# Performance work log

Measured on AMD Instinct MI355X. Metric: run time of the kernel, lower is better.

The kernel has to match this reference:

```python
import jax, jax.numpy as jnp
import numpy as np

WH, WW = 8, 8          # window_size
NUM_HEADS = 16
DIM = 512
NW = 64                # windows per image (mask leading dim)
BATCH = 16             # images
N = WH * WW            # tokens per window


def _relative_position_index():
    coords = np.stack(np.meshgrid(np.arange(WH), np.arange(WW), indexing='ij'))  # (2,Wh,Ww)
    cf = coords.reshape(2, -1)                                                   # (2,N)
    rel = cf[:, :, None] - cf[:, None, :]                                        # (2,N,N)
    rel = rel.transpose(1, 2, 0).astype(np.int64)                                # (N,N,2)
    rel[:, :, 0] += WH - 1
    rel[:, :, 1] += WW - 1
    rel[:, :, 0] *= 2 * WW - 1
    return jnp.asarray(rel.sum(-1), dtype=jnp.int32)                             # (N,N)


def setup_inputs() -> dict:
    key = jax.random.key(0)
    ks = jax.random.split(key, 8)
    B_ = BATCH * NW
    x = jax.random.normal(ks[0], (B_, N, DIM), dtype=jnp.float32)
    # 0 / -100 additive shift-style mask (Swin uses -100.0 for masked pairs)
    mraw = jax.random.uniform(ks[1], (NW, N, N))
    mask = jnp.where(mraw < 0.15, jnp.float32(-100.0), jnp.float32(0.0))
    qkv_w = jax.random.normal(ks[2], (3 * DIM, DIM), dtype=jnp.float32) * (DIM ** -0.5)
    qkv_b = jnp.zeros((3 * DIM,), dtype=jnp.float32)
    proj_w = jax.random.normal(ks[3], (DIM, DIM), dtype=jnp.float32) * (DIM ** -0.5)
    proj_b = jnp.zeros((DIM,), dtype=jnp.float32)
    n_rel = (2 * WH - 1) * (2 * WW - 1)  # 225
    rpb_table = jax.random.normal(ks[4], (n_rel, NUM_HEADS), dtype=jnp.float32) * 0.02
    rel_index = _relative_position_index()
    return {"x": x, "mask": mask, "qkv_w": qkv_w, "qkv_b": qkv_b,
            "proj_w": proj_w, "proj_b": proj_b, "rpb_table": rpb_table,
            "rel_index": rel_index}


def reference(x, mask, qkv_w, qkv_b, proj_w, proj_b, rpb_table, rel_index):
    B_, n, C = x.shape
    H = NUM_HEADS
    hd = C // H
    scale = hd ** -0.5
    qkv = x @ qkv_w.T + qkv_b                       # (B_, N, 3C)
    qkv = qkv.reshape(B_, n, 3, H, hd)
    q = qkv[:, :, 0].transpose(0, 2, 1, 3) * scale  # (B_, H, N, hd)
    k = qkv[:, :, 1].transpose(0, 2, 1, 3)
    v = qkv[:, :, 2].transpose(0, 2, 1, 3)
    attn = jnp.einsum('bhnd,bhmd->bhnm', q, k)      # (B_, H, N, N)
    bias = rpb_table[rel_index.reshape(-1)].reshape(n, n, H).transpose(2, 0, 1)  # (H,N,N)
    attn = attn + bias[None]
    nW = mask.shape[0]
    attn = attn.reshape(B_ // nW, nW, H, n, n) + mask[None, :, None]
    attn = jax.nn.softmax(attn.reshape(B_, H, n, n), axis=-1)
    out = jnp.einsum('bhnm,bhmd->bhnd', attn, v)    # (B_, H, N, hd)
    out = out.transpose(0, 2, 1, 3).reshape(B_, n, C)
    return out @ proj_w.T + proj_b
```

## Files before the change

### kernel.cpp

```cpp
#include <hip/hip_runtime.h>
#include <hip/hip_bf16.h>

typedef unsigned short u16;
typedef __attribute__((ext_vector_type(8))) short bfrag;
typedef __attribute__((ext_vector_type(4))) float ffrag;

#define NWIN_TOT 1024
#define NTOK 64
#define CDIM 512
#define NHEAD 16
#define HDIM 32
#define NW 64

__device__ __forceinline__ u16 f2bf(float f) {
  union { float f; unsigned u; } v; v.f = f;
  unsigned r = v.u + 0x7fffu + ((v.u >> 16) & 1u);
  return (u16)(r >> 16);
}

__device__ __forceinline__ float bfhi2f(unsigned hi_bits) {
  union { unsigned u; float f; } v; v.u = hi_bits; return v.f;
}

__device__ __forceinline__ ffrag mfma16(bfrag a, bfrag b, ffrag c) {
  return __builtin_amdgcn_mfma_f32_16x16x32_bf16(a, b, c, 0, 0, 0);
}

__device__ __forceinline__ void gload16(const u16* src, u16* lds) {
  __builtin_amdgcn_global_load_lds(
      (const __attribute__((address_space(1))) unsigned int*)src,
      (__attribute__((address_space(3))) unsigned int*)lds, 16, 0, 0);
}

#define BAR() __builtin_amdgcn_s_barrier()
#define SCHED0() __builtin_amdgcn_sched_barrier(0)
#define VMW(n) do { asm volatile("s_waitcnt vmcnt(" #n ")" ::: "memory"); \
                    __builtin_amdgcn_sched_barrier(0); } while (0)

__global__ __launch_bounds__(256) void k_prep(const float* __restrict__ x,
                                              const float* __restrict__ qkv_w,
                                              const float* __restrict__ proj_w,
                                              const int*   __restrict__ rel_index,
                                              const float* __restrict__ rpb,
                                              const float* __restrict__ mask,
                                              u16* __restrict__ xb,
                                              u16* __restrict__ wq, u16* __restrict__ wp,
                                              u16* __restrict__ combB) {
  int i = blockIdx.x * 256 + threadIdx.x;
  if (i < 4194304) {
    int e = i * 8;
    const float4* xp = reinterpret_cast<const float4*>(x + e);
    float4 lo = xp[0], hi = xp[1];
    union { u16 u[8]; bfrag v; } pk;
    pk.u[0] = f2bf(lo.x); pk.u[1] = f2bf(lo.y); pk.u[2] = f2bf(lo.z); pk.u[3] = f2bf(lo.w);
    pk.u[4] = f2bf(hi.x); pk.u[5] = f2bf(hi.y); pk.u[6] = f2bf(hi.z); pk.u[7] = f2bf(hi.w);
    *reinterpret_cast<bfrag*>(xb + e) = pk.v;
    return;
  }
  i -= 4194304;
  if (i < 786432) { wq[i] = f2bf(qkv_w[i]); return; }
  i -= 786432;
  if (i < 262144) { wp[i] = f2bf(proj_w[i]); return; }
  i -= 262144;
  {
    int wh = i >> 12, rc = i & 4095;
    int w0 = wh >> 4, h = wh & 15;
    combB[i] = f2bf(rpb[rel_index[rc] * 16 + h] + mask[(w0 << 12) + rc]);
  }
}

#define MFMAQ(mh, nh, BARR) \
  _Pragma("unroll") for (int i_ = 0; i_ < 4; ++i_) \
  _Pragma("unroll") for (int n_ = 0; n_ < 2; ++n_) \
  _Pragma("unroll") for (int ks_ = 0; ks_ < 2; ++ks_) \
    acc[(mh)*4+i_][(nh)*2+n_] = mfma16(a_[i_*2+ks_], BARR[n_*2+ks_], acc[(mh)*4+i_][(nh)*2+n_]);

template<int EPI>
__global__ __launch_bounds__(512, 2) void k_gemm8(const u16* __restrict__ A,
                                                  const u16* __restrict__ W,
                                                  const float* __restrict__ bias,
                                                  u16* __restrict__ qws, u16* __restrict__ kws,
                                                  u16* __restrict__ vws,
                                                  float* __restrict__ out) {
  constexpr int NT = (EPI == 0) ? 6 : 2;
  constexpr int NWG = 256 * NT;
  extern __shared__ __align__(16) u16 smem[];

  const int bid = blockIdx.x;
  const int tile = (bid & 7) * (NWG >> 3) + (bid >> 3);
  const int bn = tile % NT, bm = tile / NT;
  const int brow = bm << 8, bcol = bn << 8;

  const int tid = threadIdx.x;
  const int wv = tid >> 6, lane = tid & 63, c15 = lane & 15, g = lane >> 4;
  const int wr = wv >> 2, wc = wv & 3;
  const int rowA0 = wr * 128 + c15;
  const int rowB0 = wc * 64 + c15;
  const ffrag zf = {0.f, 0.f, 0.f, 0.f};

  ffrag acc[8][4];
#pragma unroll
  for (int i = 0; i < 8; ++i)
#pragma unroll
    for (int n = 0; n < 4; ++n) acc[i][n] = zf;

  auto stage = [&](int t, int mat, int half) {
    u16* db = smem + ((t & 1) * 2 + mat) * 16384 + half * 8192;
    const u16* gsrc = mat ? W : A;
    const int gr0 = (mat ? bcol : brow) + half * 128;
#pragma unroll
    for (int l = 0; l < 2; ++l) {
      int e = l * 4096 + tid * 8;
      int r = e >> 6, cb = (e & 63) << 1;
      int scol = (cb ^ ((r & 7) << 4)) >> 1;
      gload16(gsrc + (size_t)(gr0 + r) * 512 + t * 64 + scol, db + e);
    }
  };

  stage(0, 0, 0); stage(0, 0, 1); stage(0, 1, 0); stage(0, 1, 1);
  stage(1, 0, 0); stage(1, 0, 1); stage(1, 1, 0); stage(1, 1, 1);
  VMW(8);
  BAR();

  bfrag b0_[4];
  {
    const char* B0_ = (const char*)(smem + 1 * 16384);
#pragma unroll
    for (int n = 0; n < 2; ++n) {
      int rb = rowB0 + n * 16;
#pragma unroll
      for (int ks = 0; ks < 2; ++ks)
        b0_[n * 2 + ks] = *(const bfrag*)(B0_ + rb * 128 + ((ks * 64 + g * 16) ^ ((rb & 7) << 4)));
    }
  }

  for (int t = 0; t < 8; ++t) {
    const char* As_ = (const char*)(smem + ((t & 1) * 2 + 0) * 16384);
    const char* Bs_ = (const char*)(smem + ((t & 1) * 2 + 1) * 16384);
    bfrag a_[8], b1_[4];

#pragma unroll
    for (int i = 0; i < 4; ++i) {
      int ra = rowA0 + i * 16;
#pragma unroll
      for (int ks = 0; ks < 2; ++ks)
        a_[i * 2 + ks] = *(const bfrag*)(As_ + ra * 128 + ((ks * 64 + g * 16) ^ ((ra & 7) << 4)));
    }
    BAR();
    __builtin_amdgcn_s_setprio(1);
    MFMAQ(0, 0, b0_);
    __builtin_amdgcn_s_setprio(0);
    BAR();

#pragma unroll
    for (int n = 0; n < 2; ++n) {
      int rb = rowB0 + 32 + n * 16;
#pragma unroll
      for (int ks = 0; ks < 2; ++ks)
        b1_[n * 2 + ks] = *(const bfrag*)(Bs_ + rb * 128 + ((ks * 64 + g * 16) ^ ((rb & 7) << 4)));
    }
    BAR();
    __builtin_amdgcn_s_setprio(1);
    MFMAQ(0, 1, b1_);
    __builtin_amdgcn_s_setprio(0);
    BAR();

#pragma unroll
    for (int i = 0; i < 4; ++i) {
      int ra = rowA0 + 64 + i * 16;
#pragma unroll
      for (int ks = 0; ks < 2; ++ks)
        a_[i * 2 + ks] = *(const bfrag*)(As_ + ra * 128 + ((ks * 64 + g * 16) ^ ((ra & 7) << 4)));
    }
    SCHED0();
    if (t + 2 < 8) { stage(t + 2, 1, 0); stage(t + 2, 1, 1); }
    BAR();
    __builtin_amdgcn_s_setprio(1);
    MFMAQ(1, 1, b1_);
    __builtin_amdgcn_s_setprio(0);
    BAR();

    if (t + 2 < 8) { stage(t + 2, 0, 0); stage(t + 2, 0, 1); }
    if (t < 6) { VMW(8); } else if (t == 6) { VMW(0); }
    BAR();
    __builtin_amdgcn_s_setprio(1);
    MFMAQ(1, 0, b0_);
    __builtin_amdgcn_s_setprio(0);
    if (t < 7) {
      const char* Bn_ = (const char*)(smem + (((t + 1) & 1) * 2 + 1) * 16384);
#pragma unroll
      for (int n = 0; n < 2; ++n) {
        int rb = rowB0 + n * 16;
#pragma unroll
        for (int ks = 0; ks < 2; ++ks)
          b0_[n * 2 + ks] = *(const bfrag*)(Bn_ + rb * 128 + ((ks * 64 + g * 16) ^ ((rb & 7) << 4)));
      }
    }
    BAR();
  }

  if (EPI == 0) {
    const int which = bn >> 1;
    const int head0 = (bn & 1) * 8;
    const int win0 = brow >> 6;
    const float s = (which == 0) ? 0.17677669529663687f : 1.0f;
    u16* lds16 = smem;

#pragma unroll
    for (int n = 0; n < 4; ++n) {
      int colc = wc * 64 + n * 16 + c15;
      float bz = bias[bcol + colc];
#pragma unroll
      for (int i = 0; i < 8; ++i) {
#pragma unroll
        for (int r = 0; r < 4; ++r) {
          int row = wr * 128 + i * 16 + g * 4 + r;
          int ch = ((colc >> 3) ^ (row & 31)) & 31;
          lds16[row * 256 + (colc & 7) + (ch << 3)] = f2bf((acc[i][n][r] + bz) * s);
        }
      }
    }
    __syncthreads();

    if (which < 2) {
      u16* dst = (which == 0) ? qws : kws;
#pragma unroll
      for (int it = 0; it < 16; ++it) {
        int G = it * 512 + tid;
        int win = G >> 11, rem = G & 2047;
        int hl = rem >> 8, rem2 = rem & 255;
        int tok = rem2 >> 2, d0 = (rem2 & 3) << 3;
        int row = win * 64 + tok, col = hl * 32 + d0;
        int ch = ((col >> 3) ^ (row & 31)) & 31;
        bfrag v = *(const bfrag*)(lds16 + row * 256 + (ch << 3));
        size_t o = ((size_t)((win0 + win) * NHEAD + head0 + hl) * NTOK + tok) * HDIM + d0;
        *(bfrag*)(dst + o) = v;
      }
    } else {
#pragma unroll
      for (int it = 0; it < 16; ++it) {
        int G = it * 512 + tid;
        int win = G >> 11, rem = G & 2047;
        int hl = rem >> 8, rem2 = rem & 255;
        int d = rem2 >> 3, tok0 = (rem2 & 7) << 3;
        int col = hl * 32 + d;
        union { u16 u[8]; bfrag v; } pk;
#pragma unroll
        for (int j = 0; j < 8; ++j) {
          int row = win * 64 + tok0 + j;
          int ch = ((col >> 3) ^ (row & 31)) & 31;
          pk.u[j] = lds16[row * 256 + (col & 7) + (ch << 3)];
        }
        size_t o = ((size_t)((win0 + win) * NHEAD + head0 + hl) * HDIM + d) * NTOK + tok0;
        *(bfrag*)(vws + o) = pk.v;
      }
    }
  } else {
#pragma unroll
    for (int n = 0; n < 4; ++n) {
      int c = bcol + wc * 64 + n * 16 + c15;
      float bz = bias[c];
      float* po = out + (size_t)(brow + wr * 128) * CDIM + c;
#pragma unroll
      for (int i = 0; i < 8; ++i)
#pragma unroll
        for (int r = 0; r < 4; ++r)
          po[(size_t)(i * 16 + g * 4 + r) * CDIM] = acc[i][n][r] + bz;
    }
  }
}

__global__ __launch_bounds__(256) void k_attn(const u16* __restrict__ qws,
                                              const u16* __restrict__ kws,
                                              const u16* __restrict__ vws,
                                              const u16* __restrict__ combB,
                                              u16* __restrict__ yws) {
  __shared__ __align__(16) u16 plds[4][NTOK * NTOK];
  const int tid = threadIdx.x, w = tid >> 6, lane = tid & 63;
  const int c15 = lane & 15, g = lane >> 4, g4 = g * 4;
  const int p = blockIdx.x * 4 + w;
  const int b = p >> 4, h = p & 15;

  const u16* qb_ = qws + (size_t)p * (NTOK * HDIM);
  const u16* kb_ = kws + (size_t)p * (NTOK * HDIM);
  bfrag qa[4], ka[4];
#pragma unroll
  for (int t = 0; t < 4; ++t) {
    qa[t] = *reinterpret_cast<const bfrag*>(qb_ + (t * 16 + c15) * HDIM + g * 8);
    ka[t] = *reinterpret_cast<const bfrag*>(kb_ + (t * 16 + c15) * HDIM + g * 8);
  }

  const u16* cB = combB + ((size_t)(((b & (NW - 1)) << 4) + h) << 12);
  u16* pl = plds[w];
  const ffrag zf = {0.f, 0.f, 0.f, 0.f};

#pragma unroll
  for (int it = 0; it < 4; ++it) {
    int row = it * 16 + c15;
    float l[4][4];
    float mx = -3.0e38f;
#pragma unroll
    for (int jt = 0; jt < 4; ++jt) {
      ffrag s = mfma16(ka[jt], qa[it], zf);
      uint2 cw = *reinterpret_cast<const uint2*>(cB + row * 64 + jt * 16 + g4);
      l[jt][0] = s[0] + bfhi2f(cw.x << 16);
      l[jt][1] = s[1] + bfhi2f(cw.x & 0xffff0000u);
      l[jt][2] = s[2] + bfhi2f(cw.y << 16);
      l[jt][3] = s[3] + bfhi2f(cw.y & 0xffff0000u);
      mx = fmaxf(mx, fmaxf(fmaxf(l[jt][0], l[jt][1]), fmaxf(l[jt][2], l[jt][3])));
    }
    mx = fmaxf(mx, __shfl_xor(mx, 16));
    mx = fmaxf(mx, __shfl_xor(mx, 32));
    float sum = 0.f;
#pragma unroll
    for (int jt = 0; jt < 4; ++jt)
#pragma unroll
      for (int r = 0; r < 4; ++r) {
        float e = __expf(l[jt][r] - mx);
        l[jt][r] = e;
        sum += e;
      }
    sum += __shfl_xor(sum, 16);
    sum += __shfl_xor(sum, 32);
    float inv = 1.0f / sum;
#pragma unroll
    for (int jt = 0; jt < 4; ++jt) {
      union { u16 u[4]; uint2 v; } pk;
#pragma unroll
      for (int r = 0; r < 4; ++r) pk.u[r] = f2bf(l[jt][r] * inv);
      int off = row * 64 + ((jt * 16 + g4) ^ ((row & 7) << 3));
      *reinterpret_cast<uint2*>(&pl[off]) = pk.v;
    }
  }
  __syncthreads();

  const u16* vb_ = vws + (size_t)p * (HDIM * NTOK);
  ffrag o0[4] = {zf, zf, zf, zf}, o1[4] = {zf, zf, zf, zf};
#pragma unroll
  for (int ks = 0; ks < 2; ++ks) {
    bfrag vf0 = *reinterpret_cast<const bfrag*>(vb_ + c15 * NTOK + ks * 32 + g * 8);
    bfrag vf1 = *reinterpret_cast<const bfrag*>(vb_ + (16 + c15) * NTOK + ks * 32 + g * 8);
#pragma unroll
    for (int i = 0; i < 4; ++i) {
      int prow = i * 16 + c15;
      bfrag pa = *reinterpret_cast<const bfrag*>(
          &pl[prow * 64 + ((ks * 32 + g * 8) ^ ((prow & 7) << 3))]);
      o0[i] = mfma16(pa, vf0, o0[i]);
      o1[i] = mfma16(pa, vf1, o1[i]);
    }
  }
  __syncthreads();

  u16* yl = &plds[0][0];
#pragma unroll
  for (int i = 0; i < 4; ++i)
#pragma unroll
    for (int r = 0; r < 4; ++r) {
      int tok = i * 16 + g4 + r;
      yl[tok * 136 + w * 32 + c15] = f2bf(o0[i][r]);
      yl[tok * 136 + w * 32 + 16 + c15] = f2bf(o1[i][r]);
    }
  __syncthreads();
  {
    const int b2 = blockIdx.x >> 2;
    const int h0 = (blockIdx.x * 4) & 15;
    int row = tid >> 2, seg = tid & 3;
    const u16* src = yl + row * 136 + seg * 32;
    u16* dst = yws + ((size_t)b2 * NTOK + row) * CDIM + h0 * HDIM + seg * 32;
    bfrag v0 = *(const bfrag*)(src);
    bfrag v1 = *(const bfrag*)(src + 8);
    bfrag v2 = *(const bfrag*)(src + 16);
    bfrag v3 = *(const bfrag*)(src + 24);
    *(bfrag*)(dst) = v0;
    *(bfrag*)(dst + 8) = v1;
    *(bfrag*)(dst + 16) = v2;
    *(bfrag*)(dst + 24) = v3;
  }
}

extern "C" void kernel_launch(void* const* d_in, const int* in_sizes, int n_in,
                              void* d_out, int out_size, void* d_ws, size_t ws_size,
                              hipStream_t stream) {
  const float* x      = (const float*)d_in[0];
  const float* mask   = (const float*)d_in[1];
  const float* qkv_w  = (const float*)d_in[2];
  const float* qkv_b  = (const float*)d_in[3];
  const float* proj_w = (const float*)d_in[4];
  const float* proj_b = (const float*)d_in[5];
  const float* rpb    = (const float*)d_in[6];
  const int*   rel    = (const int*)d_in[7];
  float* out = (float*)d_out;

  char* ws = (char*)d_ws;
  constexpr size_t SZ_QKV = (size_t)NWIN_TOT * NHEAD * NTOK * HDIM * 2;
  u16* qws = (u16*)(ws);
  u16* kws = (u16*)(ws + SZ_QKV);
  u16* vws = (u16*)(ws + 2 * SZ_QKV);
  u16* xb  = (u16*)(ws + 3 * SZ_QKV);
  u16* yws = xb;
  u16* wq  = (u16*)(ws + 4 * SZ_QKV);
  u16* wp  = (u16*)(ws + 4 * SZ_QKV + 1572864);
  u16* combB = (u16*)(ws + 4 * SZ_QKV + 1572864 + 524288);

  hipFuncSetAttribute((const void*)k_gemm8<0>,
                      hipFuncAttributeMaxDynamicSharedMemorySize, 131072);
  hipFuncSetAttribute((const void*)k_gemm8<1>,
                      hipFuncAttributeMaxDynamicSharedMemorySize, 131072);

  k_prep<<<dim3(36864), dim3(256), 0, stream>>>(x, qkv_w, proj_w, rel, rpb, mask,
                                                xb, wq, wp, combB);
  k_gemm8<0><<<dim3(256 * 6), dim3(512), 131072, stream>>>(xb, wq, qkv_b, qws, kws, vws, nullptr);
  k_attn<<<dim3(NWIN_TOT * NHEAD / 4), dim3(256), 0, stream>>>(qws, kws, vws, combB, yws);
  k_gemm8<1><<<dim3(256 * 2), dim3(512), 131072, stream>>>(yws, wp, proj_b, nullptr, nullptr, nullptr, out);
}
```

Baseline: 315.7 us.

## Switch GEMMs to 256x128 tiles with triple-buffered LDS and direct epilogue

Replaces the 256x256 double-buffered GEMM with 256x128 tiles, a 3-stage LDS ring (144KB, one block per CU) and a simpler two-phase MFMA loop with fewer barriers. The QKV epilogue now writes q/k/v straight from registers to the head-major workspace layouts, dropping the LDS transpose staging. This doubles the number of workgroups and shortens per-tile work. In exchange it lowers reuse per loaded byte, and the direct epilogue uses scattered, uncoalesced 2-byte stores for q/k.

```diff
diff --git a/kernel.cpp b/kernel.cpp
--- a/kernel.cpp
+++ b/kernel.cpp
@@ -33,7 +33,6 @@
 }
 
 #define BAR() __builtin_amdgcn_s_barrier()
-#define SCHED0() __builtin_amdgcn_sched_barrier(0)
 #define VMW(n) do { asm volatile("s_waitcnt vmcnt(" #n ")" ::: "memory"); \
                     __builtin_amdgcn_sched_barrier(0); } while (0)
 
@@ -69,203 +68,147 @@
   }
 }
 
-#define MFMAQ(mh, nh, BARR) \
-  _Pragma("unroll") for (int i_ = 0; i_ < 4; ++i_) \
-  _Pragma("unroll") for (int n_ = 0; n_ < 2; ++n_) \
-  _Pragma("unroll") for (int ks_ = 0; ks_ < 2; ++ks_) \
-    acc[(mh)*4+i_][(nh)*2+n_] = mfma16(a_[i_*2+ks_], BARR[n_*2+ks_], acc[(mh)*4+i_][(nh)*2+n_]);
-
 template<int EPI>
-__global__ __launch_bounds__(512, 2) void k_gemm8(const u16* __restrict__ A,
+__global__ __launch_bounds__(512, 1) void k_gemm3(const u16* __restrict__ A,
                                                   const u16* __restrict__ W,
                                                   const float* __restrict__ bias,
                                                   u16* __restrict__ qws, u16* __restrict__ kws,
                                                   u16* __restrict__ vws,
                                                   float* __restrict__ out) {
-  constexpr int NT = (EPI == 0) ? 6 : 2;
+  constexpr int NT = (EPI == 0) ? 12 : 4;
   constexpr int NWG = 256 * NT;
   extern __shared__ __align__(16) u16 smem[];
 
   const int bid = blockIdx.x;
   const int tile = (bid & 7) * (NWG >> 3) + (bid >> 3);
   const int bn = tile % NT, bm = tile / NT;
-  const int brow = bm << 8, bcol = bn << 8;
+  const int brow = bm << 8, bcol = bn << 7;
 
   const int tid = threadIdx.x;
   const int wv = tid >> 6, lane = tid & 63, c15 = lane & 15, g = lane >> 4;
-  const int wr = wv >> 2, wc = wv & 3;
-  const int rowA0 = wr * 128 + c15;
-  const int rowB0 = wc * 64 + c15;
+  const int g4 = g * 4;
+  const int wr = wv >> 1, wc = wv & 1;
   const ffrag zf = {0.f, 0.f, 0.f, 0.f};
 
-  ffrag acc[8][4];
-#pragma unroll
-  for (int i = 0; i < 8; ++i)
+  ffrag acc[4][4];
+#pragma unroll
+  for (int i = 0; i < 4; ++i)
 #pragma unroll
     for (int n = 0; n < 4; ++n) acc[i][n] = zf;
 
-  auto stage = [&](int t, int mat, int half) {
-    u16* db = smem + ((t & 1) * 2 + mat) * 16384 + half * 8192;
-    const u16* gsrc = mat ? W : A;
-    const int gr0 = (mat ? bcol : brow) + half * 128;
+  auto stageA = [&](int t) {
+    u16* db = smem + (t % 3) * 24576;
+#pragma unroll
+    for (int l = 0; l < 4; ++l) {
+      int e = l * 4096 + tid * 8;
+      int r = e >> 6, cb = (e & 63) << 1;
+      int scol = (cb ^ ((r & 7) << 4)) >> 1;
+      gload16(A + (size_t)(brow + r) * 512 + t * 64 + scol, db + e);
+    }
+  };
+  auto stageB = [&](int t) {
+    u16* db = smem + (t % 3) * 24576 + 16384;
 #pragma unroll
     for (int l = 0; l < 2; ++l) {
       int e = l * 4096 + tid * 8;
       int r = e >> 6, cb = (e & 63) << 1;
       int scol = (cb ^ ((r & 7) << 4)) >> 1;
-      gload16(gsrc + (size_t)(gr0 + r) * 512 + t * 64 + scol, db + e);
+      gload16(W + (size_t)(bcol + r) * 512 + t * 64 + scol, db + e);
     }
   };
 
-  stage(0, 0, 0); stage(0, 0, 1); stage(0, 1, 0); stage(0, 1, 1);
-  stage(1, 0, 0); stage(1, 0, 1); stage(1, 1, 0); stage(1, 1, 1);
-  VMW(8);
+  stageA(0); stageB(0); stageA(1); stageB(1);
+  VMW(6);
   BAR();
 
-  bfrag b0_[4];
-  {
-    const char* B0_ = (const char*)(smem + 1 * 16384);
-#pragma unroll
-    for (int n = 0; n < 2; ++n) {
-      int rb = rowB0 + n * 16;
-#pragma unroll
-      for (int ks = 0; ks < 2; ++ks)
-        b0_[n * 2 + ks] = *(const bfrag*)(B0_ + rb * 128 + ((ks * 64 + g * 16) ^ ((rb & 7) << 4)));
-    }
-  }
-
   for (int t = 0; t < 8; ++t) {
-    const char* As_ = (const char*)(smem + ((t & 1) * 2 + 0) * 16384);
-    const char* Bs_ = (const char*)(smem + ((t & 1) * 2 + 1) * 16384);
-    bfrag a_[8], b1_[4];
+    const char* As_ = (const char*)(smem + (t % 3) * 24576);
+    const char* Bs_ = As_ + 32768;
+    bfrag a_[4], b_[4];
 
 #pragma unroll
     for (int i = 0; i < 4; ++i) {
-      int ra = rowA0 + i * 16;
-#pragma unroll
-      for (int ks = 0; ks < 2; ++ks)
-        a_[i * 2 + ks] = *(const bfrag*)(As_ + ra * 128 + ((ks * 64 + g * 16) ^ ((ra & 7) << 4)));
-    }
+      int ra = wr * 64 + i * 16 + c15;
+      a_[i] = *(const bfrag*)(As_ + ra * 128 + ((g * 16) ^ ((ra & 7) << 4)));
+    }
+#pragma unroll
+    for (int n = 0; n < 4; ++n) {
+      int rb = wc * 64 + n * 16 + c15;
+      b_[n] = *(const bfrag*)(Bs_ + rb * 128 + ((g * 16) ^ ((rb & 7) << 4)));
+    }
+    if (t + 2 < 8) stageA(t + 2);
     BAR();
     __builtin_amdgcn_s_setprio(1);
-    MFMAQ(0, 0, b0_);
+#pragma unroll
+    for (int i = 0; i < 4; ++i)
+#pragma unroll
+      for (int n = 0; n < 4; ++n)
+        acc[i][n] = mfma16(a_[i], b_[n], acc[i][n]);
     __builtin_amdgcn_s_setprio(0);
-    BAR();
-
-#pragma unroll
-    for (int n = 0; n < 2; ++n) {
-      int rb = rowB0 + 32 + n * 16;
-#pragma unroll
-      for (int ks = 0; ks < 2; ++ks)
-        b1_[n * 2 + ks] = *(const bfrag*)(Bs_ + rb * 128 + ((ks * 64 + g * 16) ^ ((rb & 7) << 4)));
-    }
-    BAR();
+
+#pragma unroll
+    for (int i = 0; i < 4; ++i) {
+      int ra = wr * 64 + i * 16 + c15;
+      a_[i] = *(const bfrag*)(As_ + ra * 128 + ((64 + g * 16) ^ ((ra & 7) << 4)));
+    }
+#pragma unroll
+    for (int n = 0; n < 4; ++n) {
+      int rb = wc * 64 + n * 16 + c15;
+      b_[n] = *(const bfrag*)(Bs_ + rb * 128 + ((64 + g * 16) ^ ((rb & 7) << 4)));
+    }
+    if (t + 2 < 8) stageB(t + 2);
     __builtin_amdgcn_s_setprio(1);
-    MFMAQ(0, 1, b1_);
+#pragma unroll
+    for (int i = 0; i < 4; ++i)
+#pragma unroll
+      for (int n = 0; n < 4; ++n)
+        acc[i][n] = mfma16(a_[i], b_[n], acc[i][n]);
     __builtin_amdgcn_s_setprio(0);
-    BAR();
-
-#pragma unroll
-    for (int i = 0; i < 4; ++i) {
-      int ra = rowA0 + 64 + i * 16;
-#pragma unroll
-      for (int ks = 0; ks < 2; ++ks)
-        a_[i * 2 + ks] = *(const bfrag*)(As_ + ra * 128 + ((ks * 64 + g * 16) ^ ((ra & 7) << 4)));
-    }
-    SCHED0();
-    if (t + 2 < 8) { stage(t + 2, 1, 0); stage(t + 2, 1, 1); }
-    BAR();
-    __builtin_amdgcn_s_setprio(1);
-    MFMAQ(1, 1, b1_);
-    __builtin_amdgcn_s_setprio(0);
-    BAR();
-
-    if (t + 2 < 8) { stage(t + 2, 0, 0); stage(t + 2, 0, 1); }
-    if (t < 6) { VMW(8); } else if (t == 6) { VMW(0); }
-    BAR();
-    __builtin_amdgcn_s_setprio(1);
-    MFMAQ(1, 0, b0_);
-    __builtin_amdgcn_s_setprio(0);
-    if (t < 7) {
-      const char* Bn_ = (const char*)(smem + (((t + 1) & 1) * 2 + 1) * 16384);
-#pragma unroll
-      for (int n = 0; n < 2; ++n) {
-        int rb = rowB0 + n * 16;
-#pragma unroll
-        for (int ks = 0; ks < 2; ++ks)
-          b0_[n * 2 + ks] = *(const bfrag*)(Bn_ + rb * 128 + ((ks * 64 + g * 16) ^ ((rb & 7) << 4)));
-      }
-    }
-    BAR();
+    if (t < 6) { VMW(6); BAR(); }
+    else if (t == 6) { VMW(0); BAR(); }
   }
 
   if (EPI == 0) {
-    const int which = bn >> 1;
-    const int head0 = (bn & 1) * 8;
-    const int win0 = brow >> 6;
-    const float s = (which == 0) ? 0.17677669529663687f : 1.0f;
-    u16* lds16 = smem;
-
-#pragma unroll
-    for (int n = 0; n < 4; ++n) {
-      int colc = wc * 64 + n * 16 + c15;
-      float bz = bias[bcol + colc];
-#pragma unroll
-      for (int i = 0; i < 8; ++i) {
-#pragma unroll
-        for (int r = 0; r < 4; ++r) {
-          int row = wr * 128 + i * 16 + g * 4 + r;
-          int ch = ((colc >> 3) ^ (row & 31)) & 31;
-          lds16[row * 256 + (colc & 7) + (ch << 3)] = f2bf((acc[i][n][r] + bz) * s);
-        }
-      }
-    }
-    __syncthreads();
-
-    if (which < 2) {
-      u16* dst = (which == 0) ? qws : kws;
-#pragma unroll
-      for (int it = 0; it < 16; ++it) {
-        int G = it * 512 + tid;
-        int win = G >> 11, rem = G & 2047;
-        int hl = rem >> 8, rem2 = rem & 255;
-        int tok = rem2 >> 2, d0 = (rem2 & 3) << 3;
-        int row = win * 64 + tok, col = hl * 32 + d0;
-        int ch = ((col >> 3) ^ (row & 31)) & 31;
-        bfrag v = *(const bfrag*)(lds16 + row * 256 + (ch << 3));
-        size_t o = ((size_t)((win0 + win) * NHEAD + head0 + hl) * NTOK + tok) * HDIM + d0;
-        *(bfrag*)(dst + o) = v;
-      }
-    } else {
-#pragma unroll
-      for (int it = 0; it < 16; ++it) {
-        int G = it * 512 + tid;
-        int win = G >> 11, rem = G & 2047;
-        int hl = rem >> 8, rem2 = rem & 255;
-        int d = rem2 >> 3, tok0 = (rem2 & 7) << 3;
-        int col = hl * 32 + d;
-        union { u16 u[8]; bfrag v; } pk;
-#pragma unroll
-        for (int j = 0; j < 8; ++j) {
-          int row = win * 64 + tok0 + j;
-          int ch = ((col >> 3) ^ (row & 31)) & 31;
-          pk.u[j] = lds16[row * 256 + (col & 7) + (ch << 3)];
-        }
-        size_t o = ((size_t)((win0 + win) * NHEAD + head0 + hl) * HDIM + d) * NTOK + tok0;
-        *(bfrag*)(vws + o) = pk.v;
-      }
-    }
-  } else {
+    const float SCALE = 0.17677669529663687f;
+    const int which = bn >> 2;
+    const int win = (brow >> 6) + wr;
 #pragma unroll
     for (int n = 0; n < 4; ++n) {
       int c = bcol + wc * 64 + n * 16 + c15;
       float bz = bias[c];
-      float* po = out + (size_t)(brow + wr * 128) * CDIM + c;
-#pragma unroll
-      for (int i = 0; i < 8; ++i)
+      int cq = c & 511, h = cq >> 5, d = cq & 31;
+      size_t slab = ((size_t)(win * NHEAD + h)) << 11;
+      if (which == 2) {
+        u16* vp = vws + slab + (d << 6);
+#pragma unroll
+        for (int i = 0; i < 4; ++i) {
+          int tok0 = i * 16 + g4;
+          union { u16 u[4]; uint2 v; } pk;
+#pragma unroll
+          for (int r = 0; r < 4; ++r) pk.u[r] = f2bf(acc[i][n][r] + bz);
+          *reinterpret_cast<uint2*>(vp + tok0) = pk.v;
+        }
+      } else {
+        const float s = (which == 0) ? SCALE : 1.0f;
+        u16* qp = ((which == 0) ? qws : kws) + slab + d;
+#pragma unroll
+        for (int i = 0; i < 4; ++i)
+#pragma unroll
+          for (int r = 0; r < 4; ++r)
+            qp[(i * 16 + g4 + r) << 5] = f2bf((acc[i][n][r] + bz) * s);
+      }
+    }
+  } else {
+#pragma unroll
+    for (int n = 0; n < 4; ++n) {
+      int c = bcol + wc * 64 + n * 16 + c15;
+      float bz = bias[c];
+      float* po = out + (size_t)(brow + wr * 64) * CDIM + c;
+#pragma unroll
+      for (int i = 0; i < 4; ++i)
 #pragma unroll
         for (int r = 0; r < 4; ++r)
-          po[(size_t)(i * 16 + g * 4 + r) * CDIM] = acc[i][n][r] + bz;
+          po[(size_t)(i * 16 + g4 + r) * CDIM] = acc[i][n][r] + bz;
     }
   }
 }
@@ -402,14 +345,16 @@
   u16* wp  = (u16*)(ws + 4 * SZ_QKV + 1572864);
   u16* combB = (u16*)(ws + 4 * SZ_QKV + 1572864 + 524288);
 
-  hipFuncSetAttribute((const void*)k_gemm8<0>,
-                      hipFuncAttributeMaxDynamicSharedMemorySize, 131072);
-  hipFuncSetAttribute((const void*)k_gemm8<1>,
-                      hipFuncAttributeMaxDynamicSharedMemorySize, 131072);
+  hipFuncSetAttribute((const void*)k_gemm3<0>,
+                      hipFuncAttributeMaxDynamicSharedMemorySize, 147456);
+  hipFuncSetAttribute((const void*)k_gemm3<1>,
+                      hipFuncAttributeMaxDynamicSharedMemorySize, 147456);
 
   k_prep<<<dim3(36864), dim3(256), 0, stream>>>(x, qkv_w, proj_w, rel, rpb, mask,
                                                 xb, wq, wp, combB);
-  k_gemm8<0><<<dim3(256 * 6), dim3(512), 131072, stream>>>(xb, wq, qkv_b, qws, kws, vws, nullptr);
+  k_gemm3<0><<<dim3(256 * 12), dim3(512), 147456, stream>>>(xb, wq, qkv_b,
+                                                            qws, kws, vws, nullptr);
   k_attn<<<dim3(NWIN_TOT * NHEAD / 4), dim3(256), 0, stream>>>(qws, kws, vws, combB, yws);
-  k_gemm8<1><<<dim3(256 * 2), dim3(512), 131072, stream>>>(yws, wp, proj_b, nullptr, nullptr, nullptr, out);
-}
+  k_gemm3<1><<<dim3(256 * 4), dim3(512), 147456, stream>>>(yws, wp, proj_b,
+                                                           nullptr, nullptr, nullptr, out);
+}
```

Result: slower. 324.5 us (+2.8%).
